# Kernel tuning notes

Hardware: AMD Instinct MI355X
Metric: run time of the kernel (lower is better)

The kernel has to match this reference:

```python
import jax, jax.numpy as jnp
import numpy as np

H = 4        # num_heads
R = 5        # dilation_rate
W = 49       # window_size
D = 256      # d_model // 2
B = 32
N = 4900     # must be divisible by W*R = 245


def setup_inputs() -> dict:
    key = jax.random.key(0)
    k1, k2, k3, k4, k5 = jax.random.split(key, 5)
    s = 1.0 / np.sqrt(D)
    return {
        "emb": jax.random.normal(k1, (B, N, D), dtype=jnp.float32),
        "Wq": jax.random.normal(k2, (D, D), dtype=jnp.float32) * s,
        "bq": jax.random.normal(k3, (D,), dtype=jnp.float32) * s,
        "Wo": jax.random.normal(k4, (D, D), dtype=jnp.float32) * s,
        "bo": jax.random.normal(k5, (D,), dtype=jnp.float32) * s,
    }


def reference(emb, Wq, bq, Wo, bo):
    b, n, d = emb.shape
    dh = d // H
    g = n // (W * R)  # number of segments
    # Original forward uses q_proj for q, k AND v (faithful to source bug).
    q = emb @ Wq.T + bq  # [B, N, D]
    # Dilated local windows: token index = g*(W*R) + i*R + r.
    # Tokens sharing (segment g, dilation offset r) attend densely over i in [0, W).
    x = q.reshape(b, g, W, R, H, dh)
    scale = jnp.asarray(dh, q.dtype) ** -0.5
    scores = jnp.einsum("bgirhd,bgjrhd->bgrhij", x, x) * scale  # [B,G,R,H,W,W]
    attn = jax.nn.softmax(scores, axis=-1)
    out = jnp.einsum("bgrhij,bgjrhd->bgirhd", attn, x)  # [B,G,W,R,H,dh]
    out = out.reshape(b, n, d)
    return out @ Wo.T + bo
```

## Files before the change

### kernel.cpp

```cpp
#include <hip/hip_runtime.h>
#include <hip/hip_bf16.h>
#include <math.h>

#define NH     4
#define RD     5
#define WW     49
#define DM     256
#define BATCH  32
#define NTOK   4900
#define GSEG   20
#define SEG    245

typedef short bf16x8 __attribute__((ext_vector_type(8)));
typedef short bf16x4 __attribute__((ext_vector_type(4)));
typedef float f32x4  __attribute__((ext_vector_type(4)));

__device__ __forceinline__ short f2bf(float f) {
    union { __hip_bfloat16 h; short s; } u;
    u.h = __float2bfloat16(f);
    return u.s;
}

__device__ __forceinline__ int qix(int row, int col) {
    return row * 256 + (col ^ ((row & 7) << 3));
}
__device__ __forceinline__ int xix(int d, int j) {
    return d * 64 + (j ^ ((((d >> 3) ^ d) & 7) << 3));
}
__device__ __forceinline__ int pix(int i, int j) {
    return i * 64 + (j ^ ((i & 7) << 3));
}

__global__ __launch_bounds__(256)
void wcvt(const float* __restrict__ Wq, const float* __restrict__ Wo,
          short* __restrict__ Wqb, short* __restrict__ Wob) {
    int t = blockIdx.x * 256 + threadIdx.x;
    const float* src = (t < 16384) ? Wq : Wo;
    short* dst = (t < 16384) ? Wqb : Wob;
    int i = (t & 16383) * 4;
    float4 v = *(const float4*)(src + i);
    bf16x4 o = { f2bf(v.x), f2bf(v.y), f2bf(v.z), f2bf(v.w) };
    *(bf16x4*)(dst + i) = o;
}

__global__ __launch_bounds__(512, 2)
void fused(const float* __restrict__ emb, const short* __restrict__ Wqb,
           const float* __restrict__ bq, const short* __restrict__ Wob,
           const float* __restrict__ bo, float* __restrict__ out) {
    __shared__ __align__(16) short smem[SEG * DM + 4 * 4096];
    short* q_s = smem;

    const int tid = threadIdx.x;
    const int wv = tid >> 6, ln = tid & 63, lc = ln & 15, lq = ln >> 4;
    const int b = blockIdx.x / GSEG, g = blockIdx.x % GSEG;
    const size_t ebase = ((size_t)b * NTOK + (size_t)g * SEG) * DM;

    const int wm = (wv & 3) * 64;
    const int wn = (wv >> 2) * 128;

    {
        const float* ar[4];
        const short* br[8];
        #pragma unroll
        for (int mi = 0; mi < 4; mi++) {
            int t = wm + mi * 16 + lc;
            t = (t > SEG - 1) ? (SEG - 1) : t;
            ar[mi] = emb + ebase + (size_t)t * DM + lq * 8;
        }
        #pragma unroll
        for (int ni = 0; ni < 8; ni++)
            br[ni] = Wqb + (size_t)(wn + ni * 16 + lc) * DM + lq * 8;

        f32x4 acc[4][8] = {};
        for (int k0 = 0; k0 < DM; k0 += 32) {
            bf16x8 af[4], bfr[8];
            #pragma unroll
            for (int mi = 0; mi < 4; mi++) {
                float4 v0 = *(const float4*)(ar[mi] + k0);
                float4 v1 = *(const float4*)(ar[mi] + k0 + 4);
                bf16x8 t8 = { f2bf(v0.x), f2bf(v0.y), f2bf(v0.z), f2bf(v0.w),
                              f2bf(v1.x), f2bf(v1.y), f2bf(v1.z), f2bf(v1.w) };
                af[mi] = t8;
            }
            #pragma unroll
            for (int ni = 0; ni < 8; ni++) bfr[ni] = *(const bf16x8*)(br[ni] + k0);
            #pragma unroll
            for (int mi = 0; mi < 4; mi++)
                #pragma unroll
                for (int ni = 0; ni < 8; ni++)
                    acc[mi][ni] = __builtin_amdgcn_mfma_f32_16x16x32_bf16(
                        af[mi], bfr[ni], acc[mi][ni], 0, 0, 0);
        }
        float bv[8];
        #pragma unroll
        for (int ni = 0; ni < 8; ni++) bv[ni] = bq[wn + ni * 16 + lc];
        #pragma unroll
        for (int mi = 0; mi < 4; mi++)
            #pragma unroll
            for (int rg = 0; rg < 4; rg++) {
                const int t = wm + mi * 16 + lq * 4 + rg;
                if (t < SEG) {
                    const int lr = (t % RD) * WW + t / RD;
                    #pragma unroll
                    for (int ni = 0; ni < 8; ni++)
                        q_s[qix(lr, wn + ni * 16 + lc)] =
                            f2bf(acc[mi][ni][rg] + bv[ni]);
                }
            }
    }
    __syncthreads();

    {
        const int tm = wv >> 2, tv = wv & 3, ttid = tid & 255;
        short* xt = smem + SEG * DM + tm * 4096;
        short* sp = smem + SEG * DM + 8192 + tm * 4096;
        for (int rr = 0; rr < 10; rr++) {
            const int gi = rr * 2 + tm, r = gi >> 2, c0 = (gi & 3) * 64;

            #pragma unroll
            for (int u0 = 0; u0 < 2; u0++) {
                const int u = ttid + u0 * 256, j = u >> 3, dc = (u & 7) * 8;
                bf16x8 v = (bf16x8){0, 0, 0, 0, 0, 0, 0, 0};
                if (j < WW) v = *(const bf16x8*)&q_s[qix(r * WW + j, c0 + dc)];
                #pragma unroll
                for (int e = 0; e < 8; e++) xt[xix(dc + e, j)] = v[e];
            }
            f32x4 sa[4] = {};
            {
                const int arw = r * WW + tv * 16 + lc;
                const bf16x8 a0 = *(const bf16x8*)&q_s[qix(arw, c0 + lq * 8)];
                const bf16x8 a1 = *(const bf16x8*)&q_s[qix(arw, c0 + 32 + lq * 8)];
                #pragma unroll
                for (int ni = 0; ni < 4; ni++) {
                    const int brw = r * WW + ni * 16 + lc;
                    const bf16x8 b0 = *(const bf16x8*)&q_s[qix(brw, c0 + lq * 8)];
                    const bf16x8 b1 = *(const bf16x8*)&q_s[qix(brw, c0 + 32 + lq * 8)];
                    sa[ni] = __builtin_amdgcn_mfma_f32_16x16x32_bf16(a0, b0, sa[ni], 0, 0, 0);
                    sa[ni] = __builtin_amdgcn_mfma_f32_16x16x32_bf16(a1, b1, sa[ni], 0, 0, 0);
                }
            }
            __syncthreads();

            #pragma unroll
            for (int rg = 0; rg < 4; rg++) {
                float s[4];
                float m = -1e30f;
                #pragma unroll
                for (int ni = 0; ni < 4; ni++) {
                    s[ni] = sa[ni][rg] * 0.125f;
                    if (ni * 16 + lc < WW) m = fmaxf(m, s[ni]);
                }
                m = fmaxf(m, __shfl_xor(m, 1));
                m = fmaxf(m, __shfl_xor(m, 2));
                m = fmaxf(m, __shfl_xor(m, 4));
                m = fmaxf(m, __shfl_xor(m, 8));
                float e4[4], l_ = 0.f;
                #pragma unroll
                for (int ni = 0; ni < 4; ni++) {
                    e4[ni] = (ni * 16 + lc < WW) ? __expf(s[ni] - m) : 0.f;
                    l_ += e4[ni];
                }
                l_ += __shfl_xor(l_, 1);
                l_ += __shfl_xor(l_, 2);
                l_ += __shfl_xor(l_, 4);
                l_ += __shfl_xor(l_, 8);
                const float inv = 1.f / l_;
                const int pr = tv * 16 + lq * 4 + rg;
                #pragma unroll
                for (int ni = 0; ni < 4; ni++)
                    sp[pix(pr, ni * 16 + lc)] = f2bf(e4[ni] * inv);
            }
            f32x4 oa[4] = {};
            {
                const int arw = tv * 16 + lc;
                const bf16x8 a0 = *(const bf16x8*)&sp[pix(arw, lq * 8)];
                const bf16x8 a1 = *(const bf16x8*)&sp[pix(arw, 32 + lq * 8)];
                #pragma unroll
                for (int ni = 0; ni < 4; ni++) {
                    const int d = ni * 16 + lc;
                    const bf16x8 b0 = *(const bf16x8*)&xt[xix(d, lq * 8)];
                    const bf16x8 b1 = *(const bf16x8*)&xt[xix(d, 32 + lq * 8)];
                    oa[ni] = __builtin_amdgcn_mfma_f32_16x16x32_bf16(a0, b0, oa[ni], 0, 0, 0);
                    oa[ni] = __builtin_amdgcn_mfma_f32_16x16x32_bf16(a1, b1, oa[ni], 0, 0, 0);
                }
            }
            #pragma unroll
            for (int rg = 0; rg < 4; rg++) {
                const int i = tv * 16 + lq * 4 + rg;
                if (i < WW) {
                    #pragma unroll
                    for (int ni = 0; ni < 4; ni++)
                        q_s[qix(r * WW + i, c0 + ni * 16 + lc)] = f2bf(oa[ni][rg]);
                }
            }
            __syncthreads();
        }
    }

    {
        const short* br[8];
        #pragma unroll
        for (int ni = 0; ni < 8; ni++)
            br[ni] = Wob + (size_t)(wn + ni * 16 + lc) * DM + lq * 8;
        int lr[4];
        #pragma unroll
        for (int mi = 0; mi < 4; mi++) {
            int t = wm + mi * 16 + lc;
            t = (t > SEG - 1) ? (SEG - 1) : t;
            lr[mi] = (t % RD) * WW + t / RD;
        }
        f32x4 acc[4][8] = {};
        for (int k0 = 0; k0 < DM; k0 += 32) {
            bf16x8 af[4], bfr[8];
            #pragma unroll
            for (int mi = 0; mi < 4; mi++)
                af[mi] = *(const bf16x8*)&q_s[qix(lr[mi], k0 + lq * 8)];
            #pragma unroll
            for (int ni = 0; ni < 8; ni++) bfr[ni] = *(const bf16x8*)(br[ni] + k0);
            #pragma unroll
            for (int mi = 0; mi < 4; mi++)
                #pragma unroll
                for (int ni = 0; ni < 8; ni++)
                    acc[mi][ni] = __builtin_amdgcn_mfma_f32_16x16x32_bf16(
                        af[mi], bfr[ni], acc[mi][ni], 0, 0, 0);
        }
        float bv[8];
        #pragma unroll
        for (int ni = 0; ni < 8; ni++) bv[ni] = bo[wn + ni * 16 + lc];
        #pragma unroll
        for (int mi = 0; mi < 4; mi++)
            #pragma unroll
            for (int rg = 0; rg < 4; rg++) {
                const int t = wm + mi * 16 + lq * 4 + rg;
                if (t < SEG) {
                    float* op = out + ebase + (size_t)t * DM;
                    #pragma unroll
                    for (int ni = 0; ni < 8; ni++)
                        op[wn + ni * 16 + lc] = acc[mi][ni][rg] + bv[ni];
                }
            }
    }
}

extern "C" void kernel_launch(void* const* d_in, const int* in_sizes, int n_in,
                              void* d_out, int out_size, void* d_ws, size_t ws_size,
                              hipStream_t stream) {
    const float* emb = (const float*)d_in[0];
    const float* Wq  = (const float*)d_in[1];
    const float* bq  = (const float*)d_in[2];
    const float* Wo  = (const float*)d_in[3];
    const float* bo  = (const float*)d_in[4];
    float* out = (float*)d_out;

    short* Wqb = (short*)d_ws;
    short* Wob = Wqb + DM * DM;

    wcvt<<<dim3(128), dim3(256), 0, stream>>>(Wq, Wo, Wqb, Wob);
    fused<<<dim3(BATCH * GSEG), dim3(512), 0, stream>>>(emb, Wqb, bq, Wob, bo, out);
}
```

Baseline: 467.2 us.

## Split work per dilation offset: one block per (batch, segment, r) window

Each block now handles a single 49-token dilated window (one r) instead of a full 245-token segment, giving five times as many 256-thread blocks. Each wave owns one 64-column head and does its scores, softmax and PV without the per-iteration loop and extra barriers. The projection epilogue writes both row-major and transposed copies of Q into shared memory so the PV step can read V directly. Block IDs are remapped with a stride-8 interleave. The trade-off is that every block re-reads the full Wq and Wo matrices for only 49 rows, and strided token rows reduce load coalescing.

```diff
diff --git a/kernel.cpp b/kernel.cpp
--- a/kernel.cpp
+++ b/kernel.cpp
@@ -24,11 +24,8 @@
 __device__ __forceinline__ int qix(int row, int col) {
     return row * 256 + (col ^ ((row & 7) << 3));
 }
-__device__ __forceinline__ int xix(int d, int j) {
-    return d * 64 + (j ^ ((((d >> 3) ^ d) & 7) << 3));
-}
-__device__ __forceinline__ int pix(int i, int j) {
-    return i * 64 + (j ^ ((i & 7) << 3));
+__device__ __forceinline__ int tix(int d, int j) {
+    return 64 * 256 + d * 64 + (j ^ ((d & 7) << 3));
 }
 
 __global__ __launch_bounds__(256)
@@ -43,37 +40,39 @@
     *(bf16x4*)(dst + i) = o;
 }
 
-__global__ __launch_bounds__(512, 2)
+__global__ __launch_bounds__(256, 2)
 void fused(const float* __restrict__ emb, const short* __restrict__ Wqb,
            const float* __restrict__ bq, const short* __restrict__ Wob,
            const float* __restrict__ bo, float* __restrict__ out) {
-    __shared__ __align__(16) short smem[SEG * DM + 4 * 4096];
-    short* q_s = smem;
+    __shared__ __align__(16) short sm[64 * 256 + 256 * 64];
 
     const int tid = threadIdx.x;
     const int wv = tid >> 6, ln = tid & 63, lc = ln & 15, lq = ln >> 4;
-    const int b = blockIdx.x / GSEG, g = blockIdx.x % GSEG;
-    const size_t ebase = ((size_t)b * NTOK + (size_t)g * SEG) * DM;
-
-    const int wm = (wv & 3) * 64;
-    const int wn = (wv >> 2) * 128;
+
+    const int bid = blockIdx.x;
+    const int L = (bid & 7) * 400 + (bid >> 3);
+    const int b = L / 100;
+    const int rem = L - b * 100;
+    const int g = rem / 5, r = rem - (rem / 5) * 5;
+    const size_t tok0 = (size_t)b * NTOK + (size_t)g * SEG + r;
+    const int n0 = wv * 64;
 
     {
         const float* ar[4];
-        const short* br[8];
-        #pragma unroll
-        for (int mi = 0; mi < 4; mi++) {
-            int t = wm + mi * 16 + lc;
-            t = (t > SEG - 1) ? (SEG - 1) : t;
-            ar[mi] = emb + ebase + (size_t)t * DM + lq * 8;
-        }
-        #pragma unroll
-        for (int ni = 0; ni < 8; ni++)
-            br[ni] = Wqb + (size_t)(wn + ni * 16 + lc) * DM + lq * 8;
-
-        f32x4 acc[4][8] = {};
+        const short* br[4];
+        #pragma unroll
+        for (int mi = 0; mi < 4; mi++) {
+            int t = mi * 16 + lc;
+            t = (t > WW - 1) ? (WW - 1) : t;
+            ar[mi] = emb + (tok0 + (size_t)t * RD) * DM + lq * 8;
+        }
+        #pragma unroll
+        for (int ni = 0; ni < 4; ni++)
+            br[ni] = Wqb + (size_t)(n0 + ni * 16 + lc) * DM + lq * 8;
+
+        f32x4 acc[4][4] = {};
         for (int k0 = 0; k0 < DM; k0 += 32) {
-            bf16x8 af[4], bfr[8];
+            bf16x8 af[4], bfr[4];
             #pragma unroll
             for (int mi = 0; mi < 4; mi++) {
                 float4 v0 = *(const float4*)(ar[mi] + k0);
@@ -83,71 +82,61 @@
                 af[mi] = t8;
             }
             #pragma unroll
-            for (int ni = 0; ni < 8; ni++) bfr[ni] = *(const bf16x8*)(br[ni] + k0);
+            for (int ni = 0; ni < 4; ni++) bfr[ni] = *(const bf16x8*)(br[ni] + k0);
             #pragma unroll
             for (int mi = 0; mi < 4; mi++)
                 #pragma unroll
-                for (int ni = 0; ni < 8; ni++)
+                for (int ni = 0; ni < 4; ni++)
                     acc[mi][ni] = __builtin_amdgcn_mfma_f32_16x16x32_bf16(
                         af[mi], bfr[ni], acc[mi][ni], 0, 0, 0);
         }
-        float bv[8];
-        #pragma unroll
-        for (int ni = 0; ni < 8; ni++) bv[ni] = bq[wn + ni * 16 + lc];
-        #pragma unroll
-        for (int mi = 0; mi < 4; mi++)
-            #pragma unroll
-            for (int rg = 0; rg < 4; rg++) {
-                const int t = wm + mi * 16 + lq * 4 + rg;
-                if (t < SEG) {
-                    const int lr = (t % RD) * WW + t / RD;
-                    #pragma unroll
-                    for (int ni = 0; ni < 8; ni++)
-                        q_s[qix(lr, wn + ni * 16 + lc)] =
-                            f2bf(acc[mi][ni][rg] + bv[ni]);
+        float bv[4];
+        #pragma unroll
+        for (int ni = 0; ni < 4; ni++) bv[ni] = bq[n0 + ni * 16 + lc];
+        #pragma unroll
+        for (int mi = 0; mi < 4; mi++)
+            #pragma unroll
+            for (int rg = 0; rg < 4; rg++) {
+                const int t = mi * 16 + lq * 4 + rg;
+                #pragma unroll
+                for (int ni = 0; ni < 4; ni++) {
+                    const int col = n0 + ni * 16 + lc;
+                    const short s = (t < WW) ? f2bf(acc[mi][ni][rg] + bv[ni])
+                                             : (short)0;
+                    sm[qix(t, col)] = s;
+                    sm[tix(col, t)] = s;
                 }
             }
     }
     __syncthreads();
 
     {
-        const int tm = wv >> 2, tv = wv & 3, ttid = tid & 255;
-        short* xt = smem + SEG * DM + tm * 4096;
-        short* sp = smem + SEG * DM + 8192 + tm * 4096;
-        for (int rr = 0; rr < 10; rr++) {
-            const int gi = rr * 2 + tm, r = gi >> 2, c0 = (gi & 3) * 64;
-
-            #pragma unroll
-            for (int u0 = 0; u0 < 2; u0++) {
-                const int u = ttid + u0 * 256, j = u >> 3, dc = (u & 7) * 8;
-                bf16x8 v = (bf16x8){0, 0, 0, 0, 0, 0, 0, 0};
-                if (j < WW) v = *(const bf16x8*)&q_s[qix(r * WW + j, c0 + dc)];
-                #pragma unroll
-                for (int e = 0; e < 8; e++) xt[xix(dc + e, j)] = v[e];
-            }
-            f32x4 sa[4] = {};
-            {
-                const int arw = r * WW + tv * 16 + lc;
-                const bf16x8 a0 = *(const bf16x8*)&q_s[qix(arw, c0 + lq * 8)];
-                const bf16x8 a1 = *(const bf16x8*)&q_s[qix(arw, c0 + 32 + lq * 8)];
-                #pragma unroll
-                for (int ni = 0; ni < 4; ni++) {
-                    const int brw = r * WW + ni * 16 + lc;
-                    const bf16x8 b0 = *(const bf16x8*)&q_s[qix(brw, c0 + lq * 8)];
-                    const bf16x8 b1 = *(const bf16x8*)&q_s[qix(brw, c0 + 32 + lq * 8)];
-                    sa[ni] = __builtin_amdgcn_mfma_f32_16x16x32_bf16(a0, b0, sa[ni], 0, 0, 0);
-                    sa[ni] = __builtin_amdgcn_mfma_f32_16x16x32_bf16(a1, b1, sa[ni], 0, 0, 0);
-                }
-            }
-            __syncthreads();
-
+        const int c0 = n0;
+        bf16x8 xa[4][2];
+        #pragma unroll
+        for (int mi = 0; mi < 4; mi++) {
+            xa[mi][0] = *(const bf16x8*)&sm[qix(mi * 16 + lc, c0 + lq * 8)];
+            xa[mi][1] = *(const bf16x8*)&sm[qix(mi * 16 + lc, c0 + 32 + lq * 8)];
+        }
+        f32x4 sa[4][4] = {};
+        #pragma unroll
+        for (int mi = 0; mi < 4; mi++)
+            #pragma unroll
+            for (int ni = 0; ni < 4; ni++) {
+                sa[mi][ni] = __builtin_amdgcn_mfma_f32_16x16x32_bf16(
+                    xa[mi][0], xa[ni][0], sa[mi][ni], 0, 0, 0);
+                sa[mi][ni] = __builtin_amdgcn_mfma_f32_16x16x32_bf16(
+                    xa[mi][1], xa[ni][1], sa[mi][ni], 0, 0, 0);
+            }
+        #pragma unroll
+        for (int mi = 0; mi < 4; mi++)
             #pragma unroll
             for (int rg = 0; rg < 4; rg++) {
                 float s[4];
                 float m = -1e30f;
                 #pragma unroll
                 for (int ni = 0; ni < 4; ni++) {
-                    s[ni] = sa[ni][rg] * 0.125f;
+                    s[ni] = sa[mi][ni][rg] * 0.125f;
                     if (ni * 16 + lc < WW) m = fmaxf(m, s[ni]);
                 }
                 m = fmaxf(m, __shfl_xor(m, 1));
@@ -165,78 +154,85 @@
                 l_ += __shfl_xor(l_, 4);
                 l_ += __shfl_xor(l_, 8);
                 const float inv = 1.f / l_;
-                const int pr = tv * 16 + lq * 4 + rg;
+                const int i = mi * 16 + lq * 4 + rg;
                 #pragma unroll
                 for (int ni = 0; ni < 4; ni++)
-                    sp[pix(pr, ni * 16 + lc)] = f2bf(e4[ni] * inv);
-            }
-            f32x4 oa[4] = {};
-            {
-                const int arw = tv * 16 + lc;
-                const bf16x8 a0 = *(const bf16x8*)&sp[pix(arw, lq * 8)];
-                const bf16x8 a1 = *(const bf16x8*)&sp[pix(arw, 32 + lq * 8)];
-                #pragma unroll
-                for (int ni = 0; ni < 4; ni++) {
-                    const int d = ni * 16 + lc;
-                    const bf16x8 b0 = *(const bf16x8*)&xt[xix(d, lq * 8)];
-                    const bf16x8 b1 = *(const bf16x8*)&xt[xix(d, 32 + lq * 8)];
-                    oa[ni] = __builtin_amdgcn_mfma_f32_16x16x32_bf16(a0, b0, oa[ni], 0, 0, 0);
-                    oa[ni] = __builtin_amdgcn_mfma_f32_16x16x32_bf16(a1, b1, oa[ni], 0, 0, 0);
-                }
-            }
-            #pragma unroll
-            for (int rg = 0; rg < 4; rg++) {
-                const int i = tv * 16 + lq * 4 + rg;
+                    sm[qix(i, c0 + ni * 16 + lc)] = f2bf(e4[ni] * inv);
+            }
+        bf16x8 pa[4][2], pb[4][2];
+        #pragma unroll
+        for (int mi = 0; mi < 4; mi++) {
+            pa[mi][0] = *(const bf16x8*)&sm[qix(mi * 16 + lc, c0 + lq * 8)];
+            pa[mi][1] = *(const bf16x8*)&sm[qix(mi * 16 + lc, c0 + 32 + lq * 8)];
+        }
+        #pragma unroll
+        for (int ni = 0; ni < 4; ni++) {
+            pb[ni][0] = *(const bf16x8*)&sm[tix(c0 + ni * 16 + lc, lq * 8)];
+            pb[ni][1] = *(const bf16x8*)&sm[tix(c0 + ni * 16 + lc, 32 + lq * 8)];
+        }
+        f32x4 oa[4][4] = {};
+        #pragma unroll
+        for (int mi = 0; mi < 4; mi++)
+            #pragma unroll
+            for (int ni = 0; ni < 4; ni++) {
+                oa[mi][ni] = __builtin_amdgcn_mfma_f32_16x16x32_bf16(
+                    pa[mi][0], pb[ni][0], oa[mi][ni], 0, 0, 0);
+                oa[mi][ni] = __builtin_amdgcn_mfma_f32_16x16x32_bf16(
+                    pa[mi][1], pb[ni][1], oa[mi][ni], 0, 0, 0);
+            }
+        #pragma unroll
+        for (int mi = 0; mi < 4; mi++)
+            #pragma unroll
+            for (int rg = 0; rg < 4; rg++) {
+                const int i = mi * 16 + lq * 4 + rg;
                 if (i < WW) {
                     #pragma unroll
                     for (int ni = 0; ni < 4; ni++)
-                        q_s[qix(r * WW + i, c0 + ni * 16 + lc)] = f2bf(oa[ni][rg]);
-                }
-            }
-            __syncthreads();
-        }
+                        sm[qix(i, c0 + ni * 16 + lc)] = f2bf(oa[mi][ni][rg]);
+                }
+            }
     }
+    __syncthreads();
 
     {
-        const short* br[8];
-        #pragma unroll
-        for (int ni = 0; ni < 8; ni++)
-            br[ni] = Wob + (size_t)(wn + ni * 16 + lc) * DM + lq * 8;
-        int lr[4];
-        #pragma unroll
-        for (int mi = 0; mi < 4; mi++) {
-            int t = wm + mi * 16 + lc;
-            t = (t > SEG - 1) ? (SEG - 1) : t;
-            lr[mi] = (t % RD) * WW + t / RD;
-        }
-        f32x4 acc[4][8] = {};
+        const short* br[4];
+        #pragma unroll
+        for (int ni = 0; ni < 4; ni++)
+            br[ni] = Wob + (size_t)(n0 + ni * 16 + lc) * DM + lq * 8;
+        int trow[4];
+        #pragma unroll
+        for (int mi = 0; mi < 4; mi++) {
+            int t = mi * 16 + lc;
+            trow[mi] = (t > WW - 1) ? (WW - 1) : t;
+        }
+        f32x4 acc[4][4] = {};
         for (int k0 = 0; k0 < DM; k0 += 32) {
-            bf16x8 af[4], bfr[8];
+            bf16x8 af[4], bfr[4];
             #pragma unroll
             for (int mi = 0; mi < 4; mi++)
-                af[mi] = *(const bf16x8*)&q_s[qix(lr[mi], k0 + lq * 8)];
-            #pragma unroll
-            for (int ni = 0; ni < 8; ni++) bfr[ni] = *(const bf16x8*)(br[ni] + k0);
+                af[mi] = *(const bf16x8*)&sm[qix(trow[mi], k0 + lq * 8)];
+            #pragma unroll
+            for (int ni = 0; ni < 4; ni++) bfr[ni] = *(const bf16x8*)(br[ni] + k0);
             #pragma unroll
             for (int mi = 0; mi < 4; mi++)
                 #pragma unroll
-                for (int ni = 0; ni < 8; ni++)
+                for (int ni = 0; ni < 4; ni++)
                     acc[mi][ni] = __builtin_amdgcn_mfma_f32_16x16x32_bf16(
                         af[mi], bfr[ni], acc[mi][ni], 0, 0, 0);
         }
-        float bv[8];
-        #pragma unroll
-        for (int ni = 0; ni < 8; ni++) bv[ni] = bo[wn + ni * 16 + lc];
-        #pragma unroll
-        for (int mi = 0; mi < 4; mi++)
-            #pragma unroll
-            for (int rg = 0; rg < 4; rg++) {
-                const int t = wm + mi * 16 + lq * 4 + rg;
-                if (t < SEG) {
-                    float* op = out + ebase + (size_t)t * DM;
+        float bv[4];
+        #pragma unroll
+        for (int ni = 0; ni < 4; ni++) bv[ni] = bo[n0 + ni * 16 + lc];
+        #pragma unroll
+        for (int mi = 0; mi < 4; mi++)
+            #pragma unroll
+            for (int rg = 0; rg < 4; rg++) {
+                const int t = mi * 16 + lq * 4 + rg;
+                if (t < WW) {
+                    float* op = out + (tok0 + (size_t)t * RD) * DM + n0;
                     #pragma unroll
-                    for (int ni = 0; ni < 8; ni++)
-                        op[wn + ni * 16 + lc] = acc[mi][ni][rg] + bv[ni];
+                    for (int ni = 0; ni < 4; ni++)
+                        op[ni * 16 + lc] = acc[mi][ni][rg] + bv[ni];
                 }
             }
     }
@@ -256,5 +252,6 @@
     short* Wob = Wqb + DM * DM;
 
     wcvt<<<dim3(128), dim3(256), 0, stream>>>(Wq, Wo, Wqb, Wob);
-    fused<<<dim3(BATCH * GSEG), dim3(512), 0, stream>>>(emb, Wqb, bq, Wob, bo, out);
-}
+    fused<<<dim3(BATCH * GSEG * RD), dim3(256), 0, stream>>>(
+        emb, Wqb, bq, Wob, bo, out);
+}
```

Result: no change. 473.1 us (+1.3%).
